# Kernel tuning notes

Measured on AMD Instinct MI355X. Metric: run time of the kernel, lower is better.

The kernel has to match this reference:

```python
import jax, jax.numpy as jnp
import numpy as np

N = 100000   # nodes
E = 1600000  # edges
C = 64       # hidden_channels
EPS = 1e-7   # module eps
BN_EPS = 1e-5


def setup_inputs() -> dict:
    key = jax.random.key(0)
    ks = jax.random.split(key, 6)
    x = jax.random.normal(ks[0], (N, C), jnp.float32)
    edge_index = jax.random.randint(ks[1], (2, E), 0, N)
    W1 = jax.random.normal(ks[2], (2, C, 2 * C), jnp.float32) * 0.1
    b1 = jnp.zeros((2, 2 * C), jnp.float32)
    g1 = jnp.ones((2, 2 * C), jnp.float32)
    be1 = jnp.zeros((2, 2 * C), jnp.float32)
    W2 = jax.random.normal(ks[3], (2, 2 * C, C), jnp.float32) * 0.1
    b2 = jnp.zeros((2, C), jnp.float32)
    t = jnp.ones((2,), jnp.float32)       # SoftmaxAggregation learnable temperature
    scale = jnp.ones((2,), jnp.float32)   # MessageNorm learnable scale
    bn_g = jnp.ones((2, C), jnp.float32)
    bn_b = jnp.zeros((2, C), jnp.float32)
    return dict(x=x, edge_index=edge_index, t=t, scale=scale, W1=W1, b1=b1,
                g1=g1, be1=be1, W2=W2, b2=b2, bn_g=bn_g, bn_b=bn_b)


def _batchnorm(h, g, b):
    # training-mode BatchNorm1d: biased batch statistics
    mu = h.mean(axis=0)
    var = h.var(axis=0)
    return (h - mu) * jax.lax.rsqrt(var + BN_EPS) * g + b


def _gga_conv(x, src, dst, t, scale, W1, b1, g1, be1, W2, b2):
    # message: relu(x_j) + eps  (gather over source nodes)
    msg = jax.nn.relu(x[src]) + EPS                     # [E, C]
    # segment-wise (per dst node) softmax over edges, per channel
    logits = msg * t
    m = jax.ops.segment_max(logits, dst, num_segments=N)  # [N, C]
    e = jnp.exp(logits - m[dst])
    denom = jax.ops.segment_sum(e, dst, num_segments=N)   # [N, C]
    alpha = e / denom[dst]
    agg = jax.ops.segment_sum(msg * alpha, dst, num_segments=N)  # [N, C]
    # MessageNorm(learn_scale=True): x + scale * ||x|| * normalize(agg)
    msg_n = agg / jnp.maximum(jnp.linalg.norm(agg, axis=-1, keepdims=True), 1e-12)
    x_norm = jnp.linalg.norm(x, axis=-1, keepdims=True)
    out = x + msg_n * x_norm * scale
    # MLP [C, 2C, C]: Linear -> BatchNorm -> ReLU -> Linear (plain last)
    h = jax.nn.relu(_batchnorm(out @ W1 + b1, g1, be1))
    return h @ W2 + b2


def reference(x, edge_index, t, scale, W1, b1, g1, be1, W2, b2, bn_g, bn_b):
    src, dst = edge_index[0], edge_index[1]
    intter = x
    for i in range(2):  # block_size = 2
        x = _gga_conv(x, src, dst, t[i], scale[i], W1[i], b1[i], g1[i],
                      be1[i], W2[i], b2[i])
        x = _batchnorm(x, bn_g[i], bn_b[i])
        if i < 1:
            x = jax.nn.relu(x) + EPS
    # residual + relu + eps; dropout p=0 is identity
    return jax.nn.relu(intter + x) + EPS
```

## Files before the change

### kernel.cpp

```cpp
#include <hip/hip_runtime.h>
#include <hip/hip_bf16.h>

#define C 64
#define H 128
#define FEPS 1e-7f
#define BNE 1e-5f
#define BSH 9
#define BSZ 512
#define EPB 4096

typedef __attribute__((ext_vector_type(8))) short bf16x8;
typedef __attribute__((ext_vector_type(4))) float f32x4;

__device__ __forceinline__ float us2f(ushort u) {
    unsigned int x = ((unsigned int)u) << 16;
    return __uint_as_float(x);
}
__device__ __forceinline__ ushort f2us(float f) {
    __hip_bfloat16 h = __float2bfloat16(f);
    return *reinterpret_cast<ushort*>(&h);
}

__global__ __launch_bounds__(256) void bhist_k(const int* __restrict__ dst,
                                               int* __restrict__ bucket_cnt, int E, int NB) {
    __shared__ int cnt[256];
    int tid = threadIdx.x;
    cnt[tid] = 0;
    __syncthreads();
    int base = blockIdx.x * EPB;
#pragma unroll
    for (int j = 0; j < 16; j++) {
        int e = base + tid + j * 256;
        if (e < E) atomicAdd(&cnt[dst[e] >> BSH], 1);
    }
    __syncthreads();
    if (tid < NB && cnt[tid]) atomicAdd(&bucket_cnt[tid], cnt[tid]);
}

__global__ void bscan_k(const int* __restrict__ bucket_cnt, int* __restrict__ bucket_off,
                        int* __restrict__ bucket_fill, int* __restrict__ row_start,
                        int NB, int N, int E) {
    __shared__ int s[256];
    int tid = threadIdx.x;
    int v = (tid < NB) ? bucket_cnt[tid] : 0;
    s[tid] = v;
    __syncthreads();
    for (int off = 1; off < 256; off <<= 1) {
        int t = 0;
        if (tid >= off) t = s[tid - off];
        __syncthreads();
        s[tid] += t;
        __syncthreads();
    }
    int excl = s[tid] - v;
    if (tid < NB) { bucket_off[tid] = excl; bucket_fill[tid] = excl; }
    if (tid == NB - 1) bucket_off[NB] = s[tid];
    if (tid == 0) row_start[N] = E;
}

__global__ __launch_bounds__(256) void bscat_k(const int* __restrict__ src,
                                               const int* __restrict__ dst,
                                               int* __restrict__ bucket_fill,
                                               unsigned int* __restrict__ bpak, int E) {
    __shared__ int cnt[256];
    __shared__ int sbase[256];
    int tid = threadIdx.x;
    cnt[tid] = 0;
    __syncthreads();
    int base = blockIdx.x * EPB;
    int dd[16], rk[16];
#pragma unroll
    for (int j = 0; j < 16; j++) {
        int e = base + tid + j * 256;
        dd[j] = -1;
        if (e < E) {
            int d = dst[e];
            dd[j] = d;
            rk[j] = atomicAdd(&cnt[d >> BSH], 1);
        }
    }
    __syncthreads();
    if (cnt[tid]) sbase[tid] = atomicAdd(&bucket_fill[tid], cnt[tid]);
    __syncthreads();
#pragma unroll
    for (int j = 0; j < 16; j++) {
        if (dd[j] >= 0) {
            int e = base + tid + j * 256;
            int b = dd[j] >> BSH;
            int pos = sbase[b] + rk[j];
            bpak[pos] = ((unsigned int)(dd[j] & (BSZ - 1)) << 17) | (unsigned int)src[e];
        }
    }
}

__global__ __launch_bounds__(512) void bfine_k(const int* __restrict__ bucket_off,
                                               const unsigned int* __restrict__ bpak,
                                               int* __restrict__ row_start,
                                               int* __restrict__ col, int N) {
    __shared__ int cnt[BSZ];
    __shared__ int off[BSZ];
    __shared__ int fill[BSZ];
    int tid = threadIdx.x;
    int b = blockIdx.x;
    int e0 = bucket_off[b], e1 = bucket_off[b + 1];
    int nbase = b << BSH;
    cnt[tid] = 0; fill[tid] = 0;
    __syncthreads();
    for (int e = e0 + tid; e < e1; e += 512) atomicAdd(&cnt[bpak[e] >> 17], 1);
    __syncthreads();
    int v = cnt[tid];
    off[tid] = v;
    __syncthreads();
    for (int o = 1; o < 512; o <<= 1) {
        int t = 0;
        if (tid >= o) t = off[tid - o];
        __syncthreads();
        off[tid] += t;
        __syncthreads();
    }
    int excl = off[tid] - v;
    off[tid] = excl;
    __syncthreads();
    int n = nbase + tid;
    if (n < N) row_start[n] = e0 + excl;
    for (int e = e0 + tid; e < e1; e += 512) {
        unsigned int w = bpak[e];
        int loc = w >> 17;
        int r = atomicAdd(&fill[loc], 1);
        col[e0 + off[loc] + r] = (int)(w & 0x1FFFFu);
    }
}

template <int AFF>
__global__ __launch_bounds__(256) void prep_k(const float* __restrict__ in,
                                              const float* __restrict__ fa,
                                              const float* __restrict__ fc,
                                              ushort* __restrict__ marr, int total4) {
    int i = blockIdx.x * 256 + threadIdx.x;
    if (i >= total4) return;
    float4 v = ((const float4*)in)[i];
    int c0 = (i * 4) & 63;
    float vv[4] = {v.x, v.y, v.z, v.w};
    ushort u[4];
#pragma unroll
    for (int j = 0; j < 4; j++) {
        float x = vv[j];
        if (AFF) {
            float xv = fmaxf(x * fa[c0 + j] + fc[c0 + j], 0.f) + FEPS;
            x = xv + FEPS;
        } else {
            x = fmaxf(x, 0.f) + FEPS;
        }
        u[j] = f2us(x);
    }
    ushort4 uv = make_ushort4(u[0], u[1], u[2], u[3]);
    ((ushort4*)marr)[i] = uv;
}

template <int MODE>
__global__ __launch_bounds__(256) void agg_k(const float* __restrict__ xin,
                                             const float* __restrict__ ta,
                                             const float* __restrict__ tc,
                                             const uint2* __restrict__ marr64,
                                             const int* __restrict__ rs,
                                             const int* __restrict__ col,
                                             const float* __restrict__ t,
                                             const float* __restrict__ sc,
                                             int layer, float* __restrict__ outb, int N) {
    int lane = threadIdx.x & 63;
    int wid = threadIdx.x >> 6;
    int q = lane >> 4;
    int ql = lane & 15;
    int n = blockIdx.x * 16 + wid * 4 + q;
    if (n >= N) return;
    float tv = t[layer];
    float sv = sc[layer];

    int beg = rs[n], end = rs[n + 1];
    float den[4] = {0.f, 0.f, 0.f, 0.f}, num[4] = {0.f, 0.f, 0.f, 0.f};

    auto acc4 = [&](uint2 d) {
        float m0 = __uint_as_float(d.x << 16);
        float m1 = __uint_as_float(d.x & 0xffff0000u);
        float m2 = __uint_as_float(d.y << 16);
        float m3 = __uint_as_float(d.y & 0xffff0000u);
        float e0 = __expf(m0 * tv);
        float e1 = __expf(m1 * tv);
        float e2 = __expf(m2 * tv);
        float e3 = __expf(m3 * tv);
        den[0] += e0; num[0] += m0 * e0;
        den[1] += e1; num[1] += m1 * e1;
        den[2] += e2; num[2] += m2 * e2;
        den[3] += e3; num[3] += m3 * e3;
    };

    int e = beg;
    for (; e + 8 <= end; e += 8) {
        uint2 d0 = marr64[(size_t)col[e + 0] * 16 + ql];
        uint2 d1 = marr64[(size_t)col[e + 1] * 16 + ql];
        uint2 d2 = marr64[(size_t)col[e + 2] * 16 + ql];
        uint2 d3 = marr64[(size_t)col[e + 3] * 16 + ql];
        uint2 d4 = marr64[(size_t)col[e + 4] * 16 + ql];
        uint2 d5 = marr64[(size_t)col[e + 5] * 16 + ql];
        uint2 d6 = marr64[(size_t)col[e + 6] * 16 + ql];
        uint2 d7 = marr64[(size_t)col[e + 7] * 16 + ql];
        acc4(d0); acc4(d1); acc4(d2); acc4(d3);
        acc4(d4); acc4(d5); acc4(d6); acc4(d7);
    }
    for (; e + 4 <= end; e += 4) {
        uint2 d0 = marr64[(size_t)col[e + 0] * 16 + ql];
        uint2 d1 = marr64[(size_t)col[e + 1] * 16 + ql];
        uint2 d2 = marr64[(size_t)col[e + 2] * 16 + ql];
        uint2 d3 = marr64[(size_t)col[e + 3] * 16 + ql];
        acc4(d0); acc4(d1); acc4(d2); acc4(d3);
    }
    for (; e < end; e++) {
        uint2 d0 = marr64[(size_t)col[e] * 16 + ql];
        acc4(d0);
    }

    float agg[4], aq = 0.f;
#pragma unroll
    for (int c = 0; c < 4; c++) {
        agg[c] = (den[c] > 0.f) ? (num[c] / den[c]) : 0.f;
        aq += agg[c] * agg[c];
    }

    float4 xv = ((const float4*)xin)[(size_t)n * 16 + ql];
    float xn[4];
    if (MODE == 0) {
        xn[0] = xv.x; xn[1] = xv.y; xn[2] = xv.z; xn[3] = xv.w;
    } else {
        float4 av = ((const float4*)ta)[ql];
        float4 cv = ((const float4*)tc)[ql];
        xn[0] = fmaxf(xv.x * av.x + cv.x, 0.f) + FEPS;
        xn[1] = fmaxf(xv.y * av.y + cv.y, 0.f) + FEPS;
        xn[2] = fmaxf(xv.z * av.z + cv.z, 0.f) + FEPS;
        xn[3] = fmaxf(xv.w * av.w + cv.w, 0.f) + FEPS;
    }
    float xq = xn[0] * xn[0] + xn[1] * xn[1] + xn[2] * xn[2] + xn[3] * xn[3];
    float na = aq, nx = xq;
#pragma unroll
    for (int m = 1; m <= 8; m <<= 1) {
        na += __shfl_xor(na, m, 64);
        nx += __shfl_xor(nx, m, 64);
    }
    float s = (1.0f / fmaxf(sqrtf(na), 1e-12f)) * sqrtf(nx) * sv;
    float4 o;
    o.x = xn[0] + agg[0] * s;
    o.y = xn[1] + agg[1] * s;
    o.z = xn[2] + agg[2] * s;
    o.w = xn[3] + agg[3] * s;
    ((float4*)outb)[(size_t)n * 16 + ql] = o;
}

__global__ void wprep_k(const float* __restrict__ W1, const float* __restrict__ W2,
                        ushort* __restrict__ wt1, ushort* __restrict__ wt2) {
    int idx = blockIdx.x * 256 + threadIdx.x;
    int m = idx >> 13, w = idx & 8191;
    if (m < 2) {
        int colw = w >> 6, k = w & 63;
        wt1[idx] = f2us(W1[m * 8192 + k * 128 + colw]);
    } else {
        int l = m - 2;
        int colw = w >> 7, k = w & 127;
        wt2[l * 8192 + w] = f2us(W2[l * 8192 + k * 64 + colw]);
    }
}

template <int KD, int ND, int MODE>
__global__ __launch_bounds__(256) void mlpm_k(const void* __restrict__ Ain,
                                              const float* __restrict__ fa,
                                              const float* __restrict__ fc,
                                              const ushort* __restrict__ WtT,
                                              const float* __restrict__ bias,
                                              void* __restrict__ outp,
                                              float* __restrict__ s_sum,
                                              float* __restrict__ s_ssq, int N) {
    constexpr int NT = ND / 16;
    constexpr int KS = KD / 32;
    __shared__ float ssum[ND], sssq[ND];
    int tid = threadIdx.x;
    int wave = tid >> 6, lane = tid & 63, lrow = lane & 15, kg = lane >> 4;
    if (tid < ND) { ssum[tid] = 0.f; sssq[tid] = 0.f; }
    __syncthreads();

    int base = blockIdx.x * 128;

    bf16x8 wfr[NT][KS];
#pragma unroll
    for (int t = 0; t < NT; t++)
#pragma unroll
        for (int ks = 0; ks < KS; ks++)
            wfr[t][ks] = *(const bf16x8*)(WtT + (t * 16 + lrow) * KD + ks * 32 + kg * 8);
    float bv[NT];
#pragma unroll
    for (int t = 0; t < NT; t++) bv[t] = bias[t * 16 + lrow];

    float ls[NT], lq[NT];
#pragma unroll
    for (int t = 0; t < NT; t++) { ls[t] = 0.f; lq[t] = 0.f; }

#pragma unroll
    for (int rt = 0; rt < 2; rt++) {
        int tidx = wave * 2 + rt;
        int arow = base + tidx * 16 + lrow;
        bool rok = arow < N;
        bf16x8 afr[KS];
        if (MODE == 0) {
#pragma unroll
            for (int ks = 0; ks < KS; ks++) {
                float4 v0 = make_float4(0.f, 0.f, 0.f, 0.f), v1 = v0;
                if (rok) {
                    const float4* p = (const float4*)((const float*)Ain +
                                                      (size_t)arow * KD + ks * 32 + kg * 8);
                    v0 = p[0]; v1 = p[1];
                }
                bf16x8 a;
                a[0] = (short)f2us(v0.x); a[1] = (short)f2us(v0.y);
                a[2] = (short)f2us(v0.z); a[3] = (short)f2us(v0.w);
                a[4] = (short)f2us(v1.x); a[5] = (short)f2us(v1.y);
                a[6] = (short)f2us(v1.z); a[7] = (short)f2us(v1.w);
                afr[ks] = a;
            }
        } else {
#pragma unroll
            for (int ks = 0; ks < KS; ks++) {
                int k0 = ks * 32 + kg * 8;
                uint4 v = make_uint4(0u, 0u, 0u, 0u);
                if (rok) v = *(const uint4*)((const ushort*)Ain + (size_t)arow * KD + k0);
                float4 a0 = *(const float4*)(fa + k0);
                float4 a1 = *(const float4*)(fa + k0 + 4);
                float4 c0 = *(const float4*)(fc + k0);
                float4 c1 = *(const float4*)(fc + k0 + 4);
                unsigned int w[4] = {v.x, v.y, v.z, v.w};
                float av[8] = {a0.x, a0.y, a0.z, a0.w, a1.x, a1.y, a1.z, a1.w};
                float cv[8] = {c0.x, c0.y, c0.z, c0.w, c1.x, c1.y, c1.z, c1.w};
                bf16x8 a;
#pragma unroll
                for (int p = 0; p < 4; p++) {
                    float f0 = us2f((ushort)(w[p] & 0xffffu));
                    float f1 = us2f((ushort)(w[p] >> 16));
                    f0 = fmaxf(f0 * av[2 * p] + cv[2 * p], 0.f);
                    f1 = fmaxf(f1 * av[2 * p + 1] + cv[2 * p + 1], 0.f);
                    a[2 * p] = (short)f2us(f0);
                    a[2 * p + 1] = (short)f2us(f1);
                }
                afr[ks] = a;
            }
        }
#pragma unroll
        for (int t = 0; t < NT; t++) {
            f32x4 acc = {0.f, 0.f, 0.f, 0.f};
#pragma unroll
            for (int ks = 0; ks < KS; ks++)
                acc = __builtin_amdgcn_mfma_f32_16x16x32_bf16(afr[ks], wfr[t][ks], acc, 0, 0, 0);
            int colw = t * 16 + lrow;
#pragma unroll
            for (int r = 0; r < 4; r++) {
                int orow = base + tidx * 16 + kg * 4 + r;
                float v = acc[r] + bv[t];
                if (orow < N) {
                    if (MODE == 0) ((ushort*)outp)[(size_t)orow * ND + colw] = f2us(v);
                    else ((float*)outp)[(size_t)orow * ND + colw] = v;
                    ls[t] += v; lq[t] += v * v;
                }
            }
        }
    }

#pragma unroll
    for (int t = 0; t < NT; t++) {
        float a = ls[t], b = lq[t];
        a += __shfl_xor(a, 16, 64); a += __shfl_xor(a, 32, 64);
        b += __shfl_xor(b, 16, 64); b += __shfl_xor(b, 32, 64);
        if (kg == 0) {
            atomicAdd(&ssum[t * 16 + lrow], a);
            atomicAdd(&sssq[t * 16 + lrow], b);
        }
    }
    __syncthreads();
    if (tid < ND) {
        atomicAdd(&s_sum[tid], ssum[tid]);
        atomicAdd(&s_ssq[tid], sssq[tid]);
    }
}

__global__ void bnfin_k(const float* __restrict__ sum, const float* __restrict__ ssq,
                        const float* __restrict__ g, const float* __restrict__ b,
                        float* __restrict__ a, float* __restrict__ cc, int n, float invN) {
    int i = threadIdx.x;
    if (i < n) {
        float mu = sum[i] * invN;
        float var = ssq[i] * invN - mu * mu;
        float rs = rsqrtf(var + BNE);
        float gg = g[i];
        float bb = b[i];
        a[i] = rs * gg;
        cc[i] = bb - mu * rs * gg;
    }
}

__global__ void final_k(const float4* __restrict__ x0, const float4* __restrict__ y,
                        const float* __restrict__ a2, const float* __restrict__ c2,
                        float4* __restrict__ outp, int total4) {
    int i = blockIdx.x * 256 + threadIdx.x;
    if (i >= total4) return;
    int c0 = (i * 4) & 63;
    float4 yv = y[i], xv = x0[i];
    float4 o;
    o.x = fmaxf(xv.x + yv.x * a2[c0 + 0] + c2[c0 + 0], 0.f) + FEPS;
    o.y = fmaxf(xv.y + yv.y * a2[c0 + 1] + c2[c0 + 1], 0.f) + FEPS;
    o.z = fmaxf(xv.z + yv.z * a2[c0 + 2] + c2[c0 + 2], 0.f) + FEPS;
    o.w = fmaxf(xv.w + yv.w * a2[c0 + 3] + c2[c0 + 3], 0.f) + FEPS;
    outp[i] = o;
}

extern "C" void kernel_launch(void* const* d_in, const int* in_sizes, int n_in,
                              void* d_out, int out_size, void* d_ws, size_t ws_size,
                              hipStream_t stream) {
    const float* x0 = (const float*)d_in[0];
    const int* ei = (const int*)d_in[1];
    const float* t = (const float*)d_in[2];
    const float* scale = (const float*)d_in[3];
    const float* W1 = (const float*)d_in[4];
    const float* b1 = (const float*)d_in[5];
    const float* g1 = (const float*)d_in[6];
    const float* be1 = (const float*)d_in[7];
    const float* W2 = (const float*)d_in[8];
    const float* b2 = (const float*)d_in[9];
    const float* bn_g = (const float*)d_in[10];
    const float* bn_b = (const float*)d_in[11];

    const int N = in_sizes[0] / C;
    const int E = in_sizes[1] / 2;
    const int* src = ei;
    const int* dst = ei + E;
    const int NB = (N + BSZ - 1) >> BSH;

    char* ws = (char*)d_ws;
    size_t cur = 0;
    auto alloc = [&](size_t bytes) -> char* {
        char* p = ws + cur;
        cur = (cur + bytes + 255) & ~(size_t)255;
        return p;
    };
    int* bucket_cnt = (int*)alloc(256 * 4);
    float* stats = (float*)alloc(768 * 4);
    size_t zbytes = cur;
    float* params = (float*)alloc(768 * 4);
    int* bucket_off = (int*)alloc(257 * 4);
    int* bucket_fill = (int*)alloc(256 * 4);
    int* row_start = (int*)alloc(((size_t)N + 1) * 4);
    int* col = (int*)alloc((size_t)E * 4);
    ushort* marr = (ushort*)alloc((size_t)N * C * 2);
    ushort* wt1 = (ushort*)alloc(2 * H * C * 2);
    ushort* wt2 = (ushort*)alloc(2 * C * H * 2);
    float* bout = (float*)alloc((size_t)N * C * 4);
    ushort* bh = (ushort*)alloc((size_t)N * H * 2);
    float* by = (float*)alloc((size_t)N * C * 4);
    unsigned int* bpak = (unsigned int*)bh;

    hipMemsetAsync(d_ws, 0, zbytes, stream);

    wprep_k<<<128, 256, 0, stream>>>(W1, W2, wt1, wt2);

    int nbE = (E + EPB - 1) / EPB;
    bhist_k<<<nbE, 256, 0, stream>>>(dst, bucket_cnt, E, NB);
    bscan_k<<<1, 256, 0, stream>>>(bucket_cnt, bucket_off, bucket_fill, row_start, NB, N, E);
    bscat_k<<<nbE, 256, 0, stream>>>(src, dst, bucket_fill, bpak, E);
    bfine_k<<<NB, 512, 0, stream>>>(bucket_off, bpak, row_start, col, N);

    float* sum1_0 = stats + 0;   float* ssq1_0 = stats + 128;
    float* sum2_0 = stats + 256; float* ssq2_0 = stats + 320;
    float* sum1_1 = stats + 384; float* ssq1_1 = stats + 512;
    float* sum2_1 = stats + 640; float* ssq2_1 = stats + 704;
    float* a1_0 = params + 0;   float* c1_0 = params + 128;
    float* a2_0 = params + 256; float* c2_0 = params + 320;
    float* a1_1 = params + 384; float* c1_1 = params + 512;
    float* a2_1 = params + 640; float* c2_1 = params + 704;

    const float invN = 1.0f / (float)N;
    int nbN16 = (N + 15) / 16;
    int nbT2 = (N + 127) / 128;
    int nbP = (N * C / 4 + 255) / 256;

    prep_k<0><<<nbP, 256, 0, stream>>>(x0, nullptr, nullptr, marr, N * C / 4);
    agg_k<0><<<nbN16, 256, 0, stream>>>(x0, nullptr, nullptr,
                                        (const uint2*)marr, row_start, col,
                                        t, scale, 0, bout, N);
    mlpm_k<C, H, 0><<<nbT2, 256, 0, stream>>>(bout, nullptr, nullptr, wt1, b1, bh,
                                              sum1_0, ssq1_0, N);
    bnfin_k<<<1, 128, 0, stream>>>(sum1_0, ssq1_0, g1, be1, a1_0, c1_0, H, invN);
    mlpm_k<H, C, 1><<<nbT2, 256, 0, stream>>>(bh, a1_0, c1_0, wt2, b2, by,
                                              sum2_0, ssq2_0, N);
    bnfin_k<<<1, 64, 0, stream>>>(sum2_0, ssq2_0, bn_g, bn_b, a2_0, c2_0, C, invN);

    prep_k<1><<<nbP, 256, 0, stream>>>(by, a2_0, c2_0, marr, N * C / 4);
    agg_k<1><<<nbN16, 256, 0, stream>>>(by, a2_0, c2_0,
                                        (const uint2*)marr, row_start, col,
                                        t, scale, 1, bout, N);
    mlpm_k<C, H, 0><<<nbT2, 256, 0, stream>>>(bout, nullptr, nullptr, wt1 + H * C, b1 + H, bh,
                                              sum1_1, ssq1_1, N);
    bnfin_k<<<1, 128, 0, stream>>>(sum1_1, ssq1_1, g1 + H, be1 + H, a1_1, c1_1, H, invN);
    mlpm_k<H, C, 1><<<nbT2, 256, 0, stream>>>(bh, a1_1, c1_1, wt2 + C * H, b2 + C, by,
                                              sum2_1, ssq2_1, N);
    bnfin_k<<<1, 64, 0, stream>>>(sum2_1, ssq2_1, bn_g + C, bn_b + C, a2_1, c2_1, C, invN);

    final_k<<<nbP, 256, 0, stream>>>((const float4*)x0, (const float4*)by, a2_1, c2_1,
                                     (float4*)d_out, N * C / 4);
}
```

Measured before the change: 321.9 us.

## Degree-sort nodes for aggregation, vectorize col loads, batch MLP A-loads

Adds three kernels that bucket destination nodes by in-degree and build a permutation, so each aggregation wave processes nodes with similar edge counts and suffers less load imbalance between quarter-waves. The edge loop now aligns to 4, loads column indices as int4 and prefetches the next eight before accumulating. The MLP kernel issues all A-row loads for both row tiles before any conversion, so more memory requests are in flight. Costs are three extra launches, a permuted and less coalesced output write pattern, and higher register pressure.

Result: slower. 345.9 us (+7.5%).

```diff
diff --git a/kernel.cpp b/kernel.cpp
--- a/kernel.cpp
+++ b/kernel.cpp
@@ -128,6 +128,71 @@
         int loc = w >> 17;
         int r = atomicAdd(&fill[loc], 1);
         col[e0 + off[loc] + r] = (int)(w & 0x1FFFFu);
+    }
+}
+
+__global__ __launch_bounds__(256) void dhist_k(const int* __restrict__ rs,
+                                               int* __restrict__ dbin, int N) {
+    __shared__ int h[64];
+    int tid = threadIdx.x;
+    if (tid < 64) h[tid] = 0;
+    __syncthreads();
+#pragma unroll
+    for (int j = 0; j < 4; j++) {
+        int i = blockIdx.x * 1024 + tid + j * 256;
+        if (i < N) {
+            int deg = rs[i + 1] - rs[i];
+            atomicAdd(&h[min(deg, 63)], 1);
+        }
+    }
+    __syncthreads();
+    if (tid < 64 && h[tid]) atomicAdd(&dbin[tid], h[tid]);
+}
+
+__global__ void dscan_k(const int* __restrict__ dbin, int* __restrict__ dbfill) {
+    __shared__ int s[64];
+    int tid = threadIdx.x;
+    int v = dbin[tid];
+    s[tid] = v;
+    __syncthreads();
+    for (int o = 1; o < 64; o <<= 1) {
+        int t = 0;
+        if (tid >= o) t = s[tid - o];
+        __syncthreads();
+        s[tid] += t;
+        __syncthreads();
+    }
+    dbfill[tid] = s[tid] - v;
+}
+
+__global__ __launch_bounds__(256) void dscat_k(const int* __restrict__ rs,
+                                               int* __restrict__ dbfill,
+                                               int* __restrict__ perm, int N) {
+    __shared__ int cnt[64];
+    __shared__ int sb[64];
+    int tid = threadIdx.x;
+    if (tid < 64) cnt[tid] = 0;
+    __syncthreads();
+    int bn[4], rk[4];
+#pragma unroll
+    for (int j = 0; j < 4; j++) {
+        int i = blockIdx.x * 1024 + tid + j * 256;
+        bn[j] = -1;
+        if (i < N) {
+            int deg = rs[i + 1] - rs[i];
+            bn[j] = min(deg, 63);
+            rk[j] = atomicAdd(&cnt[bn[j]], 1);
+        }
+    }
+    __syncthreads();
+    if (tid < 64 && cnt[tid]) sb[tid] = atomicAdd(&dbfill[tid], cnt[tid]);
+    __syncthreads();
+#pragma unroll
+    for (int j = 0; j < 4; j++) {
+        if (bn[j] >= 0) {
+            int i = blockIdx.x * 1024 + tid + j * 256;
+            perm[sb[bn[j]] + rk[j]] = i;
+        }
     }
 }
 
@@ -164,6 +229,7 @@
                                              const uint2* __restrict__ marr64,
                                              const int* __restrict__ rs,
                                              const int* __restrict__ col,
+                                             const int* __restrict__ perm,
                                              const float* __restrict__ t,
                                              const float* __restrict__ sc,
                                              int layer, float* __restrict__ outb, int N) {
@@ -171,8 +237,9 @@
     int wid = threadIdx.x >> 6;
     int q = lane >> 4;
     int ql = lane & 15;
-    int n = blockIdx.x * 16 + wid * 4 + q;
-    if (n >= N) return;
+    int gid = blockIdx.x * 16 + wid * 4 + q;
+    if (gid >= N) return;
+    int n = perm[gid];
     float tv = t[layer];
     float sv = sc[layer];
 
@@ -195,24 +262,34 @@
     };
 
     int e = beg;
-    for (; e + 8 <= end; e += 8) {
-        uint2 d0 = marr64[(size_t)col[e + 0] * 16 + ql];
-        uint2 d1 = marr64[(size_t)col[e + 1] * 16 + ql];
-        uint2 d2 = marr64[(size_t)col[e + 2] * 16 + ql];
-        uint2 d3 = marr64[(size_t)col[e + 3] * 16 + ql];
-        uint2 d4 = marr64[(size_t)col[e + 4] * 16 + ql];
-        uint2 d5 = marr64[(size_t)col[e + 5] * 16 + ql];
-        uint2 d6 = marr64[(size_t)col[e + 6] * 16 + ql];
-        uint2 d7 = marr64[(size_t)col[e + 7] * 16 + ql];
-        acc4(d0); acc4(d1); acc4(d2); acc4(d3);
-        acc4(d4); acc4(d5); acc4(d6); acc4(d7);
-    }
-    for (; e + 4 <= end; e += 4) {
-        uint2 d0 = marr64[(size_t)col[e + 0] * 16 + ql];
-        uint2 d1 = marr64[(size_t)col[e + 1] * 16 + ql];
-        uint2 d2 = marr64[(size_t)col[e + 2] * 16 + ql];
-        uint2 d3 = marr64[(size_t)col[e + 3] * 16 + ql];
-        acc4(d0); acc4(d1); acc4(d2); acc4(d3);
+    int head = (4 - (e & 3)) & 3;
+    if (head > end - e) head = end - e;
+    for (int i = 0; i < head; i++, e++) {
+        uint2 d0 = marr64[(size_t)col[e] * 16 + ql];
+        acc4(d0);
+    }
+    if (e + 8 <= end) {
+        int4 ca = *(const int4*)(col + e);
+        int4 cb = *(const int4*)(col + e + 4);
+        while (true) {
+            uint2 d0 = marr64[(size_t)ca.x * 16 + ql];
+            uint2 d1 = marr64[(size_t)ca.y * 16 + ql];
+            uint2 d2 = marr64[(size_t)ca.z * 16 + ql];
+            uint2 d3 = marr64[(size_t)ca.w * 16 + ql];
+            uint2 d4 = marr64[(size_t)cb.x * 16 + ql];
+            uint2 d5 = marr64[(size_t)cb.y * 16 + ql];
+            uint2 d6 = marr64[(size_t)cb.z * 16 + ql];
+            uint2 d7 = marr64[(size_t)cb.w * 16 + ql];
+            e += 8;
+            bool more = (e + 8 <= end);
+            if (more) {
+                ca = *(const int4*)(col + e);
+                cb = *(const int4*)(col + e + 4);
+            }
+            acc4(d0); acc4(d1); acc4(d2); acc4(d3);
+            acc4(d4); acc4(d5); acc4(d6); acc4(d7);
+            if (!more) break;
+        }
     }
     for (; e < end; e++) {
         uint2 d0 = marr64[(size_t)col[e] * 16 + ql];
@@ -301,39 +378,60 @@
 #pragma unroll
     for (int t = 0; t < NT; t++) { ls[t] = 0.f; lq[t] = 0.f; }
 
-#pragma unroll
-    for (int rt = 0; rt < 2; rt++) {
-        int tidx = wave * 2 + rt;
-        int arow = base + tidx * 16 + lrow;
-        bool rok = arow < N;
-        bf16x8 afr[KS];
-        if (MODE == 0) {
+    bf16x8 afr[2][KS];
+    if (MODE == 0) {
+        float4 raw[2][KS][2];
+#pragma unroll
+        for (int rt = 0; rt < 2; rt++) {
+            int arow = base + (wave * 2 + rt) * 16 + lrow;
+            bool rok = arow < N;
 #pragma unroll
             for (int ks = 0; ks < KS; ks++) {
-                float4 v0 = make_float4(0.f, 0.f, 0.f, 0.f), v1 = v0;
+                float4 z = make_float4(0.f, 0.f, 0.f, 0.f);
+                raw[rt][ks][0] = z; raw[rt][ks][1] = z;
                 if (rok) {
                     const float4* p = (const float4*)((const float*)Ain +
                                                       (size_t)arow * KD + ks * 32 + kg * 8);
-                    v0 = p[0]; v1 = p[1];
+                    raw[rt][ks][0] = p[0];
+                    raw[rt][ks][1] = p[1];
                 }
+            }
+        }
+#pragma unroll
+        for (int rt = 0; rt < 2; rt++)
+#pragma unroll
+            for (int ks = 0; ks < KS; ks++) {
+                float4 v0 = raw[rt][ks][0], v1 = raw[rt][ks][1];
                 bf16x8 a;
                 a[0] = (short)f2us(v0.x); a[1] = (short)f2us(v0.y);
                 a[2] = (short)f2us(v0.z); a[3] = (short)f2us(v0.w);
                 a[4] = (short)f2us(v1.x); a[5] = (short)f2us(v1.y);
                 a[6] = (short)f2us(v1.z); a[7] = (short)f2us(v1.w);
-                afr[ks] = a;
+                afr[rt][ks] = a;
             }
-        } else {
+    } else {
+        uint4 raw[2][KS];
+#pragma unroll
+        for (int rt = 0; rt < 2; rt++) {
+            int arow = base + (wave * 2 + rt) * 16 + lrow;
+            bool rok = arow < N;
+#pragma unroll
+            for (int ks = 0; ks < KS; ks++) {
+                raw[rt][ks] = make_uint4(0u, 0u, 0u, 0u);
+                if (rok) raw[rt][ks] = *(const uint4*)((const ushort*)Ain +
+                                                       (size_t)arow * KD + ks * 32 + kg * 8);
+            }
+        }
+#pragma unroll
+        for (int rt = 0; rt < 2; rt++)
 #pragma unroll
             for (int ks = 0; ks < KS; ks++) {
                 int k0 = ks * 32 + kg * 8;
-                uint4 v = make_uint4(0u, 0u, 0u, 0u);
-                if (rok) v = *(const uint4*)((const ushort*)Ain + (size_t)arow * KD + k0);
                 float4 a0 = *(const float4*)(fa + k0);
                 float4 a1 = *(const float4*)(fa + k0 + 4);
                 float4 c0 = *(const float4*)(fc + k0);
                 float4 c1 = *(const float4*)(fc + k0 + 4);
-                unsigned int w[4] = {v.x, v.y, v.z, v.w};
+                unsigned int w[4] = {raw[rt][ks].x, raw[rt][ks].y, raw[rt][ks].z, raw[rt][ks].w};
                 float av[8] = {a0.x, a0.y, a0.z, a0.w, a1.x, a1.y, a1.z, a1.w};
                 float cv[8] = {c0.x, c0.y, c0.z, c0.w, c1.x, c1.y, c1.z, c1.w};
                 bf16x8 a;
@@ -346,15 +444,19 @@
                     a[2 * p] = (short)f2us(f0);
                     a[2 * p + 1] = (short)f2us(f1);
                 }
-                afr[ks] = a;
+                afr[rt][ks] = a;
             }
-        }
+    }
+
+#pragma unroll
+    for (int rt = 0; rt < 2; rt++) {
+        int tidx = wave * 2 + rt;
 #pragma unroll
         for (int t = 0; t < NT; t++) {
             f32x4 acc = {0.f, 0.f, 0.f, 0.f};
 #pragma unroll
             for (int ks = 0; ks < KS; ks++)
-                acc = __builtin_amdgcn_mfma_f32_16x16x32_bf16(afr[ks], wfr[t][ks], acc, 0, 0, 0);
+                acc = __builtin_amdgcn_mfma_f32_16x16x32_bf16(afr[rt][ks], wfr[t][ks], acc, 0, 0, 0);
             int colw = t * 16 + lrow;
 #pragma unroll
             for (int r = 0; r < 4; r++) {
@@ -447,10 +549,13 @@
     };
     int* bucket_cnt = (int*)alloc(256 * 4);
     float* stats = (float*)alloc(768 * 4);
+    int* dbin = (int*)alloc(64 * 4);
     size_t zbytes = cur;
     float* params = (float*)alloc(768 * 4);
     int* bucket_off = (int*)alloc(257 * 4);
     int* bucket_fill = (int*)alloc(256 * 4);
+    int* dbfill = (int*)alloc(64 * 4);
+    int* perm = (int*)alloc((size_t)N * 4);
     int* row_start = (int*)alloc(((size_t)N + 1) * 4);
     int* col = (int*)alloc((size_t)E * 4);
     ushort* marr = (ushort*)alloc((size_t)N * C * 2);
@@ -471,6 +576,11 @@
     bscat_k<<<nbE, 256, 0, stream>>>(src, dst, bucket_fill, bpak, E);
     bfine_k<<<NB, 512, 0, stream>>>(bucket_off, bpak, row_start, col, N);
 
+    int nbD = (N + 1023) / 1024;
+    dhist_k<<<nbD, 256, 0, stream>>>(row_start, dbin, N);
+    dscan_k<<<1, 64, 0, stream>>>(dbin, dbfill);
+    dscat_k<<<nbD, 256, 0, stream>>>(row_start, dbfill, perm, N);
+
     float* sum1_0 = stats + 0;   float* ssq1_0 = stats + 128;
     float* sum2_0 = stats + 256; float* ssq2_0 = stats + 320;
     float* sum1_1 = stats + 384; float* ssq1_1 = stats + 512;
@@ -487,7 +597,7 @@
 
     prep_k<0><<<nbP, 256, 0, stream>>>(x0, nullptr, nullptr, marr, N * C / 4);
     agg_k<0><<<nbN16, 256, 0, stream>>>(x0, nullptr, nullptr,
-                                        (const uint2*)marr, row_start, col,
+                                        (const uint2*)marr, row_start, col, perm,
                                         t, scale, 0, bout, N);
     mlpm_k<C, H, 0><<<nbT2, 256, 0, stream>>>(bout, nullptr, nullptr, wt1, b1, bh,
                                               sum1_0, ssq1_0, N);
@@ -498,7 +608,7 @@
 
     prep_k<1><<<nbP, 256, 0, stream>>>(by, a2_0, c2_0, marr, N * C / 4);
     agg_k<1><<<nbN16, 256, 0, stream>>>(by, a2_0, c2_0,
-                                        (const uint2*)marr, row_start, col,
+                                        (const uint2*)marr, row_start, col, perm,
                                         t, scale, 1, bout, N);
     mlpm_k<C, H, 0><<<nbT2, 256, 0, stream>>>(bout, nullptr, nullptr, wt1 + H * C, b1 + H, bh,
                                               sum1_1, ssq1_1, N);
```
